# Kernel tuning notes

Measured on AMD Instinct MI355X. Metric: run time of the kernel, lower is better.

## Reference

```python
import jax, jax.numpy as jnp
import numpy as np

B, T, D = 2, 128, 1024
H, R, Dk, Dv = 8, 8, 64, 64


def setup_inputs() -> dict:
    key = jax.random.key(0)
    ks = jax.random.split(key, 11)
    w = lambda k, shp: jax.random.normal(k, shp, dtype=jnp.float32) * 0.02
    return {
        "hidden_states": jax.random.normal(ks[0], (B, T, D), dtype=jnp.float32),
        "Wq": w(ks[1], (D, H * Dk)),
        "Wk": w(ks[2], (D, H * Dk)),
        "Wv": w(ks[3], (D, H * Dv)),
        "Wb": w(ks[4], (D, H * R)),
        "Wtg": w(ks[5], (D, H * R)),
        "mode_logits": jax.random.normal(ks[6], (H, R), dtype=jnp.float32) * 0.1,
        "log_decay": jax.random.normal(ks[7], (H, R), dtype=jnp.float32) * 0.1,
        "omega_log_scale": jax.random.normal(ks[8], (H, R), dtype=jnp.float32) * 0.1,
        "Wg": w(ks[9], (D, H * Dv)),
        "Wo": w(ks[10], (H * Dv, D)),
    }


def _forward(x, Wq, Wk, Wv, Wb, Wtg, mode_logits, log_decay, omega_log_scale, Wg, Wo):
    b, t, _ = x.shape
    # projections
    q = (x @ Wq).reshape(b, t, H, Dk)
    k = (x @ Wk).reshape(b, t, H, Dk)
    v = (x @ Wv).reshape(b, t, H, Dv)
    beta = jax.nn.sigmoid((x @ Wb).reshape(b, t, H, R))
    tg = jax.nn.sigmoid((x @ Wtg).reshape(b, t, H, R))
    # spectral mode parameters
    pair_idx = jnp.arange(0, Dk, 2, dtype=jnp.float32)
    inv_freq = 1.0 / (10000.0 ** (pair_idx / Dk))            # [Dk/2]
    omega = jnp.exp(omega_log_scale)[..., None] * inv_freq    # [H,R,Dk/2]
    omega_full = jnp.repeat(omega, 2, axis=-1)                # [H,R,Dk] (repeat_interleave)
    cos_w = jnp.cos(omega_full)[None, :, :, None, :]          # [1,H,R,1,Dk]
    sin_w = jnp.sin(omega_full)[None, :, :, None, :]
    rho = jnp.exp(-jax.nn.softplus(log_decay))                # [H,R]
    mode_w = jax.nn.softmax(mode_logits, axis=-1)             # [H,R]

    # time-major for scan
    qT = jnp.moveaxis(q, 1, 0)
    kT = jnp.moveaxis(k, 1, 0)
    vT = jnp.moveaxis(v, 1, 0)
    betaT = jnp.moveaxis(beta, 1, 0)
    tgT = jnp.moveaxis(tg, 1, 0)

    def step(carry, xs):
        sr, si = carry                      # [B,H,R,Dv,Dk] each
        q_t, k_t, v_t, b_t, g_t = xs
        decay = (g_t * rho)[..., None, None]            # [B,H,R,1,1]
        rot_r = decay * (cos_w * sr - sin_w * si)
        rot_i = decay * (sin_w * sr + cos_w * si)
        pred = jnp.einsum('bhrvk,bhk->bhrv', rot_r, k_t)
        err = v_t[:, :, None, :] - pred                  # [B,H,R,Dv]
        write = err[..., None] * k_t[:, :, None, None, :]
        sr_new = rot_r + b_t[..., None, None] * write
        read = jnp.einsum('bhrvk,bhk->bhrv', sr_new, q_t)
        y = jnp.einsum('bhrv,hr->bhv', read, mode_w)     # [B,H,Dv]
        return (sr_new, rot_i), y

    s0 = jnp.zeros((b, H, R, Dv, Dk), dtype=x.dtype)
    _, ys = jax.lax.scan(step, (s0, s0), (qT, kT, vT, betaT, tgT))
    o = jnp.moveaxis(ys, 0, 1)                           # [B,T,H,Dv]
    gate = jax.nn.sigmoid((x @ Wg).reshape(b, t, H, Dv))
    o = (o * gate).reshape(b, t, H * Dv)
    return o @ Wo


def reference(hidden_states, Wq, Wk, Wv, Wb, Wtg, mode_logits, log_decay,
              omega_log_scale, Wg, Wo):
    return _forward(hidden_states, Wq, Wk, Wv, Wb, Wtg, mode_logits,
                    log_decay, omega_log_scale, Wg, Wo)
```

## Files before the change

kernel.cpp:

```cpp
#include <hip/hip_runtime.h>
#include <math.h>

#define T_ 128
#define NPROJ 2176
#define CH 32

typedef __attribute__((ext_vector_type(8))) short short8;
typedef __attribute__((ext_vector_type(4))) float float4v;
typedef __attribute__((ext_vector_type(2))) float float2v;

__device__ __forceinline__ ushort f2bf(float x) {
    unsigned u = __float_as_uint(x);
    u += 0x7FFF + ((u >> 16) & 1);
    return (ushort)(u >> 16);
}

__global__ __launch_bounds__(256) void prep_kernel(
    const float* __restrict__ x,
    const float* __restrict__ Wq, const float* __restrict__ Wk,
    const float* __restrict__ Wv, const float* __restrict__ Wb,
    const float* __restrict__ Wtg, const float* __restrict__ Wg,
    const float* __restrict__ Wo,
    const float* __restrict__ mode_logits, const float* __restrict__ log_decay,
    const float* __restrict__ ols,
    float* __restrict__ cosw, float* __restrict__ sinw,
    float* __restrict__ rho, float* __restrict__ modew,
    ushort* __restrict__ xb, ushort* __restrict__ wtb, ushort* __restrict__ wotb,
    float* __restrict__ Acomb)
{
    __shared__ ushort tile[64][68];
    const int blk = blockIdx.x, tid = threadIdx.x;
    if (blk < 16) {
        int idx = blk * 256 + tid;
        if (idx >= 64 * 64) return;
        int t = idx >> 6;
        int k = idx & 63;
        int h = t >> 3;
        if (k == 0) {
            float ld = log_decay[t];
            rho[t] = 1.0f / (1.0f + expf(ld));
            float m = -1e30f;
            for (int i = 0; i < 8; i++) m = fmaxf(m, mode_logits[h * 8 + i]);
            float sum = 0.0f;
            for (int i = 0; i < 8; i++) sum += expf(mode_logits[h * 8 + i] - m);
            modew[t] = expf(mode_logits[t] - m) / sum;
        }
        float osc = expf(ols[t]);
        int p = k >> 1;
        float invf = expf(-((float)(2 * p) / 64.0f) * logf(10000.0f));
        float w = osc * invf;
        cosw[idx] = cosf(w);
        sinw[idx] = sinf(w);
        return;
    }
    if (blk < 80) {
        int base = (blk - 16) * 4096 + tid * 16;
        float4 f0 = *(const float4*)&x[base];
        float4 f1 = *(const float4*)&x[base + 4];
        float4 f2 = *(const float4*)&x[base + 8];
        float4 f3 = *(const float4*)&x[base + 12];
        short8 o0, o1;
        o0[0]=f2bf(f0.x); o0[1]=f2bf(f0.y); o0[2]=f2bf(f0.z); o0[3]=f2bf(f0.w);
        o0[4]=f2bf(f1.x); o0[5]=f2bf(f1.y); o0[6]=f2bf(f1.z); o0[7]=f2bf(f1.w);
        o1[0]=f2bf(f2.x); o1[1]=f2bf(f2.y); o1[2]=f2bf(f2.z); o1[3]=f2bf(f2.w);
        o1[4]=f2bf(f3.x); o1[5]=f2bf(f3.y); o1[6]=f2bf(f3.z); o1[7]=f2bf(f3.w);
        *(short8*)&xb[base] = o0;
        *(short8*)&xb[base + 8] = o1;
        return;
    }
    if (blk >= 752) {
        int base = (blk - 752) * 4096 + tid * 16;
        float4 z = make_float4(0.f, 0.f, 0.f, 0.f);
        *(float4*)&Acomb[base] = z;
        *(float4*)&Acomb[base + 4] = z;
        *(float4*)&Acomb[base + 8] = z;
        *(float4*)&Acomb[base + 12] = z;
        return;
    }
    const float* src; int ld, c0, n0, k0, ldd; ushort* dst;
    if (blk < 624) {
        int b3 = blk - 80; int nt = b3 >> 4, kt = b3 & 15;
        n0 = nt * 64; k0 = kt * 64;
        if (n0 < 512)       { src = Wq;  c0 = n0;        ld = 512; }
        else if (n0 < 1024) { src = Wk;  c0 = n0 - 512;  ld = 512; }
        else if (n0 < 1536) { src = Wv;  c0 = n0 - 1024; ld = 512; }
        else if (n0 < 1600) { src = Wb;  c0 = n0 - 1536; ld = 64;  }
        else if (n0 < 1664) { src = Wtg; c0 = n0 - 1600; ld = 64;  }
        else                { src = Wg;  c0 = n0 - 1664; ld = 512; }
        dst = wtb; ldd = 1024;
    } else {
        int b4 = blk - 624; int nt = b4 >> 3, kt = b4 & 7;
        n0 = nt * 64; k0 = kt * 64;
        src = Wo; c0 = n0; ld = 1024; dst = wotb; ldd = 512;
    }
    #pragma unroll
    for (int rep = 0; rep < 4; rep++) {
        int k = rep * 16 + (tid >> 4);
        int nc = (tid & 15) * 4;
        float4 f = *(const float4*)&src[(size_t)(k0 + k) * ld + c0 + nc];
        tile[nc + 0][k] = f2bf(f.x);
        tile[nc + 1][k] = f2bf(f.y);
        tile[nc + 2][k] = f2bf(f.z);
        tile[nc + 3][k] = f2bf(f.w);
    }
    __syncthreads();
    #pragma unroll
    for (int rep = 0; rep < 4; rep++) {
        int n = rep * 16 + (tid >> 4);
        int kc = (tid & 15) * 4;
        uint2 u = *(const uint2*)&tile[n][kc];
        *(uint2*)&dst[(size_t)(n0 + n) * ldd + k0 + kc] = u;
    }
}

__global__ __launch_bounds__(256, 2) void proj_mfma(const ushort* __restrict__ Ab,
        const ushort* __restrict__ BTb, float* __restrict__ proj)
{
    __shared__ ushort sA[2][64][40];
    __shared__ ushort sB[2][64][40];
    const int n0 = blockIdx.x * 64, m0 = blockIdx.y * 64;
    const int tid = threadIdx.x;
    const int lane = tid & 63, w = tid >> 6;
    const int wm = w & 1, wn = w >> 1;
    const int l16 = lane & 15, quad = lane >> 4;
    const int srow = tid >> 2, skq = (tid & 3) * 8;
    const ushort* Ag = Ab + (size_t)(m0 + srow) * 1024 + skq;
    const ushort* Bg = BTb + (size_t)(n0 + srow) * 1024 + skq;
    short8 ra = *(const short8*)Ag;
    short8 rb = *(const short8*)Bg;
    float4v acc00 = {0,0,0,0}, acc01 = {0,0,0,0}, acc10 = {0,0,0,0}, acc11 = {0,0,0,0};
    for (int kt = 0; kt < 32; kt++) {
        const int cb = kt & 1;
        *(short8*)&sA[cb][srow][skq] = ra;
        *(short8*)&sB[cb][srow][skq] = rb;
        __syncthreads();
        if (kt + 1 < 32) {
            ra = *(const short8*)(Ag + (kt + 1) * 32);
            rb = *(const short8*)(Bg + (kt + 1) * 32);
        }
        short8 a0 = *(const short8*)&sA[cb][wm * 32 + l16][quad * 8];
        short8 a1 = *(const short8*)&sA[cb][wm * 32 + 16 + l16][quad * 8];
        short8 b0 = *(const short8*)&sB[cb][wn * 32 + l16][quad * 8];
        short8 b1 = *(const short8*)&sB[cb][wn * 32 + 16 + l16][quad * 8];
        acc00 = __builtin_amdgcn_mfma_f32_16x16x32_bf16(a0, b0, acc00, 0, 0, 0);
        acc01 = __builtin_amdgcn_mfma_f32_16x16x32_bf16(a0, b1, acc01, 0, 0, 0);
        acc10 = __builtin_amdgcn_mfma_f32_16x16x32_bf16(a1, b0, acc10, 0, 0, 0);
        acc11 = __builtin_amdgcn_mfma_f32_16x16x32_bf16(a1, b1, acc11, 0, 0, 0);
    }
    const bool sig = (n0 >= 1536);
    const int colb = n0 + wn * 32 + l16;
    const int rowb = m0 + wm * 32 + quad * 4;
    #pragma unroll
    for (int r2 = 0; r2 < 4; r2++) {
        float v00 = acc00[r2], v01 = acc01[r2], v10 = acc10[r2], v11 = acc11[r2];
        if (sig) {
            v00 = 1.0f / (1.0f + expf(-v00));
            v01 = 1.0f / (1.0f + expf(-v01));
            v10 = 1.0f / (1.0f + expf(-v10));
            v11 = 1.0f / (1.0f + expf(-v11));
        }
        proj[(size_t)(rowb + r2) * NPROJ + colb] = v00;
        proj[(size_t)(rowb + r2) * NPROJ + colb + 16] = v01;
        proj[(size_t)(rowb + 16 + r2) * NPROJ + colb] = v10;
        proj[(size_t)(rowb + 16 + r2) * NPROJ + colb + 16] = v11;
    }
}

template<int CTRL>
__device__ __forceinline__ float dpp_add(float x) {
    int xi = __float_as_int(x);
    int yi = __builtin_amdgcn_update_dpp(xi, xi, CTRL, 0xF, 0xF, false);
    return x + __int_as_float(yi);
}

__global__ __launch_bounds__(256, 2) void scan_kernel(const float* __restrict__ proj,
        const float* __restrict__ cosw, const float* __restrict__ sinw,
        const float* __restrict__ rho, const float* __restrict__ modew,
        float* __restrict__ Acomb)
{
    __shared__ float qk[2][CH][128];
    __shared__ float vbuf[2][CH][16];
    __shared__ float gbuf[2][CH][16];
    __shared__ float sc4[2][CH][4];

    const int bi = blockIdx.x;
    const int s  = bi & 3;
    const int hr = (bi >> 2) & 63;
    const int b  = bi >> 8;
    const int h = hr >> 3, r = hr & 7;
    const int tid = threadIdx.x;
    const int vl = tid >> 4;
    const int kl = tid & 15;

    float2v cw0, cw1, sw0, sw1;
    cw0.x = cosw[hr * 64 + kl * 4 + 0]; cw0.y = cosw[hr * 64 + kl * 4 + 1];
    cw1.x = cosw[hr * 64 + kl * 4 + 2]; cw1.y = cosw[hr * 64 + kl * 4 + 3];
    sw0.x = sinw[hr * 64 + kl * 4 + 0]; sw0.y = sinw[hr * 64 + kl * 4 + 1];
    sw1.x = sinw[hr * 64 + kl * 4 + 2]; sw1.y = sinw[hr * 64 + kl * 4 + 3];
    const float rho_hr = rho[hr];
    const float mw = modew[hr];
    float2v sr0 = {0,0}, sr1 = {0,0}, si0 = {0,0}, si1 = {0,0};

    const float* pb = proj + (size_t)b * T_ * NPROJ;
    const int qbase = h * 64;
    const int kbase = 512 + h * 64;
    const int vbase = 1024 + h * 64 + s * 16;
    const int gbase = 1664 + h * 64 + s * 16;
    const int boff  = 1536 + h * 8 + r;
    const int goff  = 1600 + h * 8 + r;

    auto stage = [&](int t0, int nb) {
        #pragma unroll
        for (int rep = 0; rep < 4; rep++) {
            int idx = rep * 256 + tid;
            int t = idx >> 5, sub = idx & 31;
            const float* row = pb + (size_t)(t0 + t) * NPROJ;
            float4 val = *(const float4*)(row + (sub < 16 ? qbase + sub * 4
                                                          : kbase + (sub - 16) * 4));
            *(float4*)&qk[nb][t][sub * 4] = val;
        }
        if (tid < 128) {
            int t = tid >> 2, sub = tid & 3;
            *(float4*)&vbuf[nb][t][sub * 4] =
                *(const float4*)(pb + (size_t)(t0 + t) * NPROJ + vbase + sub * 4);
        } else {
            int t = (tid - 128) >> 2, sub = tid & 3;
            *(float4*)&gbuf[nb][t][sub * 4] =
                *(const float4*)(pb + (size_t)(t0 + t) * NPROJ + gbase + sub * 4);
        }
        if (tid < CH)            sc4[nb][tid][0]      = pb[(size_t)(t0 + tid) * NPROJ + boff];
        else if (tid < 2 * CH)   sc4[nb][tid - CH][1] = pb[(size_t)(t0 + tid - CH) * NPROJ + goff];
    };

    stage(0, 0);
    __syncthreads();

    float* dst = Acomb + ((size_t)b * 128) * 512 + h * 64 + s * 16 + vl;

    for (int c = 0; c < T_ / CH; c++) {
        const int cb = c & 1;
        {
            int t = tid >> 3, j = tid & 7;
            float4 ka = *(const float4*)&qk[cb][t][64 + j * 8];
            float4 kb4 = *(const float4*)&qk[cb][t][64 + j * 8 + 4];
            float4 qa = *(const float4*)&qk[cb][t][j * 8];
            float4 qb4 = *(const float4*)&qk[cb][t][j * 8 + 4];
            float p = ka.x * qa.x + ka.y * qa.y + ka.z * qa.z + ka.w * qa.w
                    + kb4.x * qb4.x + kb4.y * qb4.y + kb4.z * qb4.z + kb4.w * qb4.w;
            p = dpp_add<0xB1>(p);
            p = dpp_add<0x4E>(p);
            p = dpp_add<0x141>(p);
            if (j == 0) sc4[cb][t][2] = p;
        }
        __syncthreads();
        if (c + 1 < T_ / CH) stage((c + 1) * CH, (c + 1) & 1);

        #pragma unroll 4
        for (int t = 0; t < CH; t++) {
            float4 kf = *(const float4*)&qk[cb][t][64 + kl * 4];
            float4 qf = *(const float4*)&qk[cb][t][kl * 4];
            float4 sv = *(const float4*)&sc4[cb][t][0];
            const float vv = vbuf[cb][t][vl];
            const float gate = gbuf[cb][t][vl];

            const float decay = sv.y * rho_hr;
            float2v k0; k0.x = kf.x; k0.y = kf.y;
            float2v k1; k1.x = kf.z; k1.y = kf.w;
            float2v q0; q0.x = qf.x; q0.y = qf.y;
            float2v q1; q1.x = qf.z; q1.y = qf.w;

            float2v t1 = cw0 * sr0 - sw0 * si0;
            float2v u1 = sw0 * sr0 + cw0 * si0;
            float2v t2 = cw1 * sr1 - sw1 * si1;
            float2v u2 = sw1 * sr1 + cw1 * si1;
            float2v d2; d2.x = decay; d2.y = decay;
            float2v rr0 = d2 * t1, rr1 = d2 * t2;
            si0 = d2 * u1; si1 = d2 * u2;

            float2v pk2 = rr0 * k0 + rr1 * k1;
            float2v pq2 = rr0 * q0 + rr1 * q1;
            float pk = pk2.x + pk2.y;
            float pq = pq2.x + pq2.y;
            pk = dpp_add<0xB1>(pk);  pq = dpp_add<0xB1>(pq);
            pk = dpp_add<0x4E>(pk);  pq = dpp_add<0x4E>(pq);
            pk = dpp_add<0x141>(pk); pq = dpp_add<0x141>(pq);
            pk = dpp_add<0x140>(pk); pq = dpp_add<0x140>(pq);

            const float sc = sv.x * (vv - pk);
            float2v sc2; sc2.x = sc; sc2.y = sc;
            sr0 = rr0 + sc2 * k0;
            sr1 = rr1 + sc2 * k1;
            const float rp = pq + sc * sv.z;
            if (kl == 0) atomicAdd(dst + (size_t)(c * CH + t) * 512, mw * rp * gate);
        }
        __syncthreads();
    }
}

__global__ __launch_bounds__(256, 2) void out_mfma(const float* __restrict__ Af,
        const ushort* __restrict__ BTb, float* __restrict__ C)
{
    __shared__ ushort sA[2][64][40];
    __shared__ ushort sB[2][64][40];
    const int n0 = blockIdx.x * 64, m0 = blockIdx.y * 64;
    const int tid = threadIdx.x;
    const int lane = tid & 63, w = tid >> 6;
    const int wm = w & 1, wn = w >> 1;
    const int l16 = lane & 15, quad = lane >> 4;
    const int srow = tid >> 2, skq = (tid & 3) * 8;
    const float* Ag = Af + (size_t)(m0 + srow) * 512 + skq;
    const ushort* Bg = BTb + (size_t)(n0 + srow) * 512 + skq;
    float4 fa0 = *(const float4*)Ag;
    float4 fa1 = *(const float4*)(Ag + 4);
    short8 rb = *(const short8*)Bg;
    float4v acc00 = {0,0,0,0}, acc01 = {0,0,0,0}, acc10 = {0,0,0,0}, acc11 = {0,0,0,0};
    for (int kt = 0; kt < 16; kt++) {
        const int cb = kt & 1;
        short8 ra;
        ra[0]=f2bf(fa0.x); ra[1]=f2bf(fa0.y); ra[2]=f2bf(fa0.z); ra[3]=f2bf(fa0.w);
        ra[4]=f2bf(fa1.x); ra[5]=f2bf(fa1.y); ra[6]=f2bf(fa1.z); ra[7]=f2bf(fa1.w);
        *(short8*)&sA[cb][srow][skq] = ra;
        *(short8*)&sB[cb][srow][skq] = rb;
        __syncthreads();
        if (kt + 1 < 16) {
            fa0 = *(const float4*)(Ag + (kt + 1) * 32);
            fa1 = *(const float4*)(Ag + (kt + 1) * 32 + 4);
            rb = *(const short8*)(Bg + (kt + 1) * 32);
        }
        short8 a0 = *(const short8*)&sA[cb][wm * 32 + l16][quad * 8];
        short8 a1 = *(const short8*)&sA[cb][wm * 32 + 16 + l16][quad * 8];
        short8 b0 = *(const short8*)&sB[cb][wn * 32 + l16][quad * 8];
        short8 b1 = *(const short8*)&sB[cb][wn * 32 + 16 + l16][quad * 8];
        acc00 = __builtin_amdgcn_mfma_f32_16x16x32_bf16(a0, b0, acc00, 0, 0, 0);
        acc01 = __builtin_amdgcn_mfma_f32_16x16x32_bf16(a0, b1, acc01, 0, 0, 0);
        acc10 = __builtin_amdgcn_mfma_f32_16x16x32_bf16(a1, b0, acc10, 0, 0, 0);
        acc11 = __builtin_amdgcn_mfma_f32_16x16x32_bf16(a1, b1, acc11, 0, 0, 0);
    }
    const int colb = n0 + wn * 32 + l16;
    const int rowb = m0 + wm * 32 + quad * 4;
    #pragma unroll
    for (int r2 = 0; r2 < 4; r2++) {
        C[(size_t)(rowb + r2) * 1024 + colb] = acc00[r2];
        C[(size_t)(rowb + r2) * 1024 + colb + 16] = acc01[r2];
        C[(size_t)(rowb + 16 + r2) * 1024 + colb] = acc10[r2];
        C[(size_t)(rowb + 16 + r2) * 1024 + colb + 16] = acc11[r2];
    }
}

extern "C" void kernel_launch(void* const* d_in, const int* in_sizes, int n_in,
                              void* d_out, int out_size, void* d_ws, size_t ws_size,
                              hipStream_t stream) {
    const float* x   = (const float*)d_in[0];
    const float* Wq  = (const float*)d_in[1];
    const float* Wk  = (const float*)d_in[2];
    const float* Wv  = (const float*)d_in[3];
    const float* Wb  = (const float*)d_in[4];
    const float* Wtg = (const float*)d_in[5];
    const float* ml  = (const float*)d_in[6];
    const float* ldc = (const float*)d_in[7];
    const float* ols = (const float*)d_in[8];
    const float* Wg  = (const float*)d_in[9];
    const float* Wo  = (const float*)d_in[10];
    float* out = (float*)d_out;

    float* ws = (float*)d_ws;
    float* proj    = ws;
    float* cosw    = proj + 256 * NPROJ;
    float* sinw    = cosw + 4096;
    float* rho     = sinw + 4096;
    float* modew   = rho + 64;
    ushort* xb     = (ushort*)(modew + 64);
    ushort* wotb   = (ushort*)((float*)xb + 131072);
    float*  Acomb  = (float*)wotb + 262144;
    ushort* wtb    = (ushort*)(Acomb + 131072);

    prep_kernel<<<784, 256, 0, stream>>>(x, Wq, Wk, Wv, Wb, Wtg, Wg, Wo,
                                         ml, ldc, ols, cosw, sinw, rho, modew,
                                         xb, wtb, wotb, Acomb);
    proj_mfma<<<dim3(34, 4), 256, 0, stream>>>(xb, wtb, proj);
    scan_kernel<<<512, 256, 0, stream>>>(proj, cosw, sinw, rho, modew, Acomb);
    out_mfma<<<dim3(16, 4), 256, 0, stream>>>(Acomb, wotb, out);
}
```

Baseline: 140.2 us.

## Fuse four kernels into one cooperative persistent kernel with grid syncs

```diff
diff --git a/kernel.cpp b/kernel.cpp
--- a/kernel.cpp
+++ b/kernel.cpp
@@ -1,5 +1,8 @@
 #include <hip/hip_runtime.h>
+#include <hip/hip_cooperative_groups.h>
 #include <math.h>
+
+namespace cg = cooperative_groups;
 
 #define T_ 128
 #define NPROJ 2176
@@ -13,157 +16,6 @@
     unsigned u = __float_as_uint(x);
     u += 0x7FFF + ((u >> 16) & 1);
     return (ushort)(u >> 16);
-}
-
-__global__ __launch_bounds__(256) void prep_kernel(
-    const float* __restrict__ x,
-    const float* __restrict__ Wq, const float* __restrict__ Wk,
-    const float* __restrict__ Wv, const float* __restrict__ Wb,
-    const float* __restrict__ Wtg, const float* __restrict__ Wg,
-    const float* __restrict__ Wo,
-    const float* __restrict__ mode_logits, const float* __restrict__ log_decay,
-    const float* __restrict__ ols,
-    float* __restrict__ cosw, float* __restrict__ sinw,
-    float* __restrict__ rho, float* __restrict__ modew,
-    ushort* __restrict__ xb, ushort* __restrict__ wtb, ushort* __restrict__ wotb,
-    float* __restrict__ Acomb)
-{
-    __shared__ ushort tile[64][68];
-    const int blk = blockIdx.x, tid = threadIdx.x;
-    if (blk < 16) {
-        int idx = blk * 256 + tid;
-        if (idx >= 64 * 64) return;
-        int t = idx >> 6;
-        int k = idx & 63;
-        int h = t >> 3;
-        if (k == 0) {
-            float ld = log_decay[t];
-            rho[t] = 1.0f / (1.0f + expf(ld));
-            float m = -1e30f;
-            for (int i = 0; i < 8; i++) m = fmaxf(m, mode_logits[h * 8 + i]);
-            float sum = 0.0f;
-            for (int i = 0; i < 8; i++) sum += expf(mode_logits[h * 8 + i] - m);
-            modew[t] = expf(mode_logits[t] - m) / sum;
-        }
-        float osc = expf(ols[t]);
-        int p = k >> 1;
-        float invf = expf(-((float)(2 * p) / 64.0f) * logf(10000.0f));
-        float w = osc * invf;
-        cosw[idx] = cosf(w);
-        sinw[idx] = sinf(w);
-        return;
-    }
-    if (blk < 80) {
-        int base = (blk - 16) * 4096 + tid * 16;
-        float4 f0 = *(const float4*)&x[base];
-        float4 f1 = *(const float4*)&x[base + 4];
-        float4 f2 = *(const float4*)&x[base + 8];
-        float4 f3 = *(const float4*)&x[base + 12];
-        short8 o0, o1;
-        o0[0]=f2bf(f0.x); o0[1]=f2bf(f0.y); o0[2]=f2bf(f0.z); o0[3]=f2bf(f0.w);
-        o0[4]=f2bf(f1.x); o0[5]=f2bf(f1.y); o0[6]=f2bf(f1.z); o0[7]=f2bf(f1.w);
-        o1[0]=f2bf(f2.x); o1[1]=f2bf(f2.y); o1[2]=f2bf(f2.z); o1[3]=f2bf(f2.w);
-        o1[4]=f2bf(f3.x); o1[5]=f2bf(f3.y); o1[6]=f2bf(f3.z); o1[7]=f2bf(f3.w);
-        *(short8*)&xb[base] = o0;
-        *(short8*)&xb[base + 8] = o1;
-        return;
-    }
-    if (blk >= 752) {
-        int base = (blk - 752) * 4096 + tid * 16;
-        float4 z = make_float4(0.f, 0.f, 0.f, 0.f);
-        *(float4*)&Acomb[base] = z;
-        *(float4*)&Acomb[base + 4] = z;
-        *(float4*)&Acomb[base + 8] = z;
-        *(float4*)&Acomb[base + 12] = z;
-        return;
-    }
-    const float* src; int ld, c0, n0, k0, ldd; ushort* dst;
-    if (blk < 624) {
-        int b3 = blk - 80; int nt = b3 >> 4, kt = b3 & 15;
-        n0 = nt * 64; k0 = kt * 64;
-        if (n0 < 512)       { src = Wq;  c0 = n0;        ld = 512; }
-        else if (n0 < 1024) { src = Wk;  c0 = n0 - 512;  ld = 512; }
-        else if (n0 < 1536) { src = Wv;  c0 = n0 - 1024; ld = 512; }
-        else if (n0 < 1600) { src = Wb;  c0 = n0 - 1536; ld = 64;  }
-        else if (n0 < 1664) { src = Wtg; c0 = n0 - 1600; ld = 64;  }
-        else                { src = Wg;  c0 = n0 - 1664; ld = 512; }
-        dst = wtb; ldd = 1024;
-    } else {
-        int b4 = blk - 624; int nt = b4 >> 3, kt = b4 & 7;
-        n0 = nt * 64; k0 = kt * 64;
-        src = Wo; c0 = n0; ld = 1024; dst = wotb; ldd = 512;
-    }
-    #pragma unroll
-    for (int rep = 0; rep < 4; rep++) {
-        int k = rep * 16 + (tid >> 4);
-        int nc = (tid & 15) * 4;
-        float4 f = *(const float4*)&src[(size_t)(k0 + k) * ld + c0 + nc];
-        tile[nc + 0][k] = f2bf(f.x);
-        tile[nc + 1][k] = f2bf(f.y);
-        tile[nc + 2][k] = f2bf(f.z);
-        tile[nc + 3][k] = f2bf(f.w);
-    }
-    __syncthreads();
-    #pragma unroll
-    for (int rep = 0; rep < 4; rep++) {
-        int n = rep * 16 + (tid >> 4);
-        int kc = (tid & 15) * 4;
-        uint2 u = *(const uint2*)&tile[n][kc];
-        *(uint2*)&dst[(size_t)(n0 + n) * ldd + k0 + kc] = u;
-    }
-}
-
-__global__ __launch_bounds__(256, 2) void proj_mfma(const ushort* __restrict__ Ab,
-        const ushort* __restrict__ BTb, float* __restrict__ proj)
-{
-    __shared__ ushort sA[2][64][40];
-    __shared__ ushort sB[2][64][40];
-    const int n0 = blockIdx.x * 64, m0 = blockIdx.y * 64;
-    const int tid = threadIdx.x;
-    const int lane = tid & 63, w = tid >> 6;
-    const int wm = w & 1, wn = w >> 1;
-    const int l16 = lane & 15, quad = lane >> 4;
-    const int srow = tid >> 2, skq = (tid & 3) * 8;
-    const ushort* Ag = Ab + (size_t)(m0 + srow) * 1024 + skq;
-    const ushort* Bg = BTb + (size_t)(n0 + srow) * 1024 + skq;
-    short8 ra = *(const short8*)Ag;
-    short8 rb = *(const short8*)Bg;
-    float4v acc00 = {0,0,0,0}, acc01 = {0,0,0,0}, acc10 = {0,0,0,0}, acc11 = {0,0,0,0};
-    for (int kt = 0; kt < 32; kt++) {
-        const int cb = kt & 1;
-        *(short8*)&sA[cb][srow][skq] = ra;
-        *(short8*)&sB[cb][srow][skq] = rb;
-        __syncthreads();
-        if (kt + 1 < 32) {
-            ra = *(const short8*)(Ag + (kt + 1) * 32);
-            rb = *(const short8*)(Bg + (kt + 1) * 32);
-        }
-        short8 a0 = *(const short8*)&sA[cb][wm * 32 + l16][quad * 8];
-        short8 a1 = *(const short8*)&sA[cb][wm * 32 + 16 + l16][quad * 8];
-        short8 b0 = *(const short8*)&sB[cb][wn * 32 + l16][quad * 8];
-        short8 b1 = *(const short8*)&sB[cb][wn * 32 + 16 + l16][quad * 8];
-        acc00 = __builtin_amdgcn_mfma_f32_16x16x32_bf16(a0, b0, acc00, 0, 0, 0);
-        acc01 = __builtin_amdgcn_mfma_f32_16x16x32_bf16(a0, b1, acc01, 0, 0, 0);
-        acc10 = __builtin_amdgcn_mfma_f32_16x16x32_bf16(a1, b0, acc10, 0, 0, 0);
-        acc11 = __builtin_amdgcn_mfma_f32_16x16x32_bf16(a1, b1, acc11, 0, 0, 0);
-    }
-    const bool sig = (n0 >= 1536);
-    const int colb = n0 + wn * 32 + l16;
-    const int rowb = m0 + wm * 32 + quad * 4;
-    #pragma unroll
-    for (int r2 = 0; r2 < 4; r2++) {
-        float v00 = acc00[r2], v01 = acc01[r2], v10 = acc10[r2], v11 = acc11[r2];
-        if (sig) {
-            v00 = 1.0f / (1.0f + expf(-v00));
-            v01 = 1.0f / (1.0f + expf(-v01));
-            v10 = 1.0f / (1.0f + expf(-v10));
-            v11 = 1.0f / (1.0f + expf(-v11));
-        }
-        proj[(size_t)(rowb + r2) * NPROJ + colb] = v00;
-        proj[(size_t)(rowb + r2) * NPROJ + colb + 16] = v01;
-        proj[(size_t)(rowb + 16 + r2) * NPROJ + colb] = v10;
-        proj[(size_t)(rowb + 16 + r2) * NPROJ + colb + 16] = v11;
-    }
 }
 
 template<int CTRL>
@@ -173,211 +25,347 @@
     return x + __int_as_float(yi);
 }
 
-__global__ __launch_bounds__(256, 2) void scan_kernel(const float* __restrict__ proj,
-        const float* __restrict__ cosw, const float* __restrict__ sinw,
-        const float* __restrict__ rho, const float* __restrict__ modew,
-        float* __restrict__ Acomb)
+struct KParams {
+    const float *x, *Wq, *Wk, *Wv, *Wb, *Wtg, *ml, *ldc, *ols, *Wg, *Wo;
+    float *cosw, *sinw, *rho, *modew, *proj, *Acomb, *out;
+    ushort *xb, *wtb, *wotb;
+};
+
+struct SmemGemm { ushort sA[2][64][40]; ushort sB[2][64][40]; };
+struct SmemScan { float qk[2][CH][128]; float vbuf[2][CH][16];
+                  float gbuf[2][CH][16]; float sc4[2][CH][4]; };
+struct SmemPrep { ushort tile[64][68]; };
+union Smem { SmemGemm g; SmemScan s; SmemPrep p; };
+
+__global__ __launch_bounds__(256, 2) void mega_kernel(KParams P)
 {
-    __shared__ float qk[2][CH][128];
-    __shared__ float vbuf[2][CH][16];
-    __shared__ float gbuf[2][CH][16];
-    __shared__ float sc4[2][CH][4];
-
-    const int bi = blockIdx.x;
-    const int s  = bi & 3;
-    const int hr = (bi >> 2) & 63;
-    const int b  = bi >> 8;
-    const int h = hr >> 3, r = hr & 7;
+    __shared__ Smem sm;
+    cg::grid_group grid = cg::this_grid();
+    const int blk = blockIdx.x;
     const int tid = threadIdx.x;
-    const int vl = tid >> 4;
-    const int kl = tid & 15;
-
-    float2v cw0, cw1, sw0, sw1;
-    cw0.x = cosw[hr * 64 + kl * 4 + 0]; cw0.y = cosw[hr * 64 + kl * 4 + 1];
-    cw1.x = cosw[hr * 64 + kl * 4 + 2]; cw1.y = cosw[hr * 64 + kl * 4 + 3];
-    sw0.x = sinw[hr * 64 + kl * 4 + 0]; sw0.y = sinw[hr * 64 + kl * 4 + 1];
-    sw1.x = sinw[hr * 64 + kl * 4 + 2]; sw1.y = sinw[hr * 64 + kl * 4 + 3];
-    const float rho_hr = rho[hr];
-    const float mw = modew[hr];
-    float2v sr0 = {0,0}, sr1 = {0,0}, si0 = {0,0}, si1 = {0,0};
-
-    const float* pb = proj + (size_t)b * T_ * NPROJ;
-    const int qbase = h * 64;
-    const int kbase = 512 + h * 64;
-    const int vbase = 1024 + h * 64 + s * 16;
-    const int gbase = 1664 + h * 64 + s * 16;
-    const int boff  = 1536 + h * 8 + r;
-    const int goff  = 1600 + h * 8 + r;
-
-    auto stage = [&](int t0, int nb) {
+
+    for (int u = blk; u < 784; u += 512) {
+        __syncthreads();
+        if (u < 16) {
+            int idx = u * 256 + tid;
+            if (idx < 64 * 64) {
+                int t = idx >> 6;
+                int k = idx & 63;
+                int h = t >> 3;
+                if (k == 0) {
+                    float ld = P.ldc[t];
+                    P.rho[t] = 1.0f / (1.0f + expf(ld));
+                    float m = -1e30f;
+                    for (int i = 0; i < 8; i++) m = fmaxf(m, P.ml[h * 8 + i]);
+                    float sum = 0.0f;
+                    for (int i = 0; i < 8; i++) sum += expf(P.ml[h * 8 + i] - m);
+                    P.modew[t] = expf(P.ml[t] - m) / sum;
+                }
+                float osc = expf(P.ols[t]);
+                int p = k >> 1;
+                float invf = expf(-((float)(2 * p) / 64.0f) * logf(10000.0f));
+                float w = osc * invf;
+                P.cosw[idx] = cosf(w);
+                P.sinw[idx] = sinf(w);
+            }
+        } else if (u < 80) {
+            int base = (u - 16) * 4096 + tid * 16;
+            float4 f0 = *(const float4*)&P.x[base];
+            float4 f1 = *(const float4*)&P.x[base + 4];
+            float4 f2 = *(const float4*)&P.x[base + 8];
+            float4 f3 = *(const float4*)&P.x[base + 12];
+            short8 o0, o1;
+            o0[0]=f2bf(f0.x); o0[1]=f2bf(f0.y); o0[2]=f2bf(f0.z); o0[3]=f2bf(f0.w);
+            o0[4]=f2bf(f1.x); o0[5]=f2bf(f1.y); o0[6]=f2bf(f1.z); o0[7]=f2bf(f1.w);
+            o1[0]=f2bf(f2.x); o1[1]=f2bf(f2.y); o1[2]=f2bf(f2.z); o1[3]=f2bf(f2.w);
+            o1[4]=f2bf(f3.x); o1[5]=f2bf(f3.y); o1[6]=f2bf(f3.z); o1[7]=f2bf(f3.w);
+            *(short8*)&P.xb[base] = o0;
+            *(short8*)&P.xb[base + 8] = o1;
+        } else if (u < 752) {
+            const float* src; int ld, c0, n0, k0, ldd; ushort* dst;
+            if (u < 624) {
+                int b3 = u - 80; int nt = b3 >> 4, kt = b3 & 15;
+                n0 = nt * 64; k0 = kt * 64;
+                if (n0 < 512)       { src = P.Wq;  c0 = n0;        ld = 512; }
+                else if (n0 < 1024) { src = P.Wk;  c0 = n0 - 512;  ld = 512; }
+                else if (n0 < 1536) { src = P.Wv;  c0 = n0 - 1024; ld = 512; }
+                else if (n0 < 1600) { src = P.Wb;  c0 = n0 - 1536; ld = 64;  }
+                else if (n0 < 1664) { src = P.Wtg; c0 = n0 - 1600; ld = 64;  }
+                else                { src = P.Wg;  c0 = n0 - 1664; ld = 512; }
+                dst = P.wtb; ldd = 1024;
+            } else {
+                int b4 = u - 624; int nt = b4 >> 3, kt = b4 & 7;
+                n0 = nt * 64; k0 = kt * 64;
+                src = P.Wo; c0 = n0; ld = 1024; dst = P.wotb; ldd = 512;
+            }
+            #pragma unroll
+            for (int rep = 0; rep < 4; rep++) {
+                int k = rep * 16 + (tid >> 4);
+                int nc = (tid & 15) * 4;
+                float4 f = *(const float4*)&src[(size_t)(k0 + k) * ld + c0 + nc];
+                sm.p.tile[nc + 0][k] = f2bf(f.x);
+                sm.p.tile[nc + 1][k] = f2bf(f.y);
+                sm.p.tile[nc + 2][k] = f2bf(f.z);
+                sm.p.tile[nc + 3][k] = f2bf(f.w);
+            }
+            __syncthreads();
+            #pragma unroll
+            for (int rep = 0; rep < 4; rep++) {
+                int n = rep * 16 + (tid >> 4);
+                int kc = (tid & 15) * 4;
+                uint2 uu = *(const uint2*)&sm.p.tile[n][kc];
+                *(uint2*)&dst[(size_t)(n0 + n) * ldd + k0 + kc] = uu;
+            }
+        } else {
+            int base = (u - 752) * 4096 + tid * 16;
+            float4 z = make_float4(0.f, 0.f, 0.f, 0.f);
+            *(float4*)&P.Acomb[base] = z;
+            *(float4*)&P.Acomb[base + 4] = z;
+            *(float4*)&P.Acomb[base + 8] = z;
+            *(float4*)&P.Acomb[base + 12] = z;
+        }
+    }
+    grid.sync();
+
+    if (blk < 136) {
+        const int n0 = (blk % 34) * 64, m0 = (blk / 34) * 64;
+        const int lane = tid & 63, w = tid >> 6;
+        const int wm = w & 1, wn = w >> 1;
+        const int l16 = lane & 15, quad = lane >> 4;
+        const int srow = tid >> 2, skq = (tid & 3) * 8;
+        const ushort* Ag = P.xb + (size_t)(m0 + srow) * 1024 + skq;
+        const ushort* Bg = P.wtb + (size_t)(n0 + srow) * 1024 + skq;
+        short8 ra = *(const short8*)Ag;
+        short8 rb = *(const short8*)Bg;
+        float4v acc00 = {0,0,0,0}, acc01 = {0,0,0,0}, acc10 = {0,0,0,0}, acc11 = {0,0,0,0};
+        for (int kt = 0; kt < 32; kt++) {
+            const int cb = kt & 1;
+            *(short8*)&sm.g.sA[cb][srow][skq] = ra;
+            *(short8*)&sm.g.sB[cb][srow][skq] = rb;
+            __syncthreads();
+            if (kt + 1 < 32) {
+                ra = *(const short8*)(Ag + (kt + 1) * 32);
+                rb = *(const short8*)(Bg + (kt + 1) * 32);
+            }
+            short8 a0 = *(const short8*)&sm.g.sA[cb][wm * 32 + l16][quad * 8];
+            short8 a1 = *(const short8*)&sm.g.sA[cb][wm * 32 + 16 + l16][quad * 8];
+            short8 b0 = *(const short8*)&sm.g.sB[cb][wn * 32 + l16][quad * 8];
+            short8 b1 = *(const short8*)&sm.g.sB[cb][wn * 32 + 16 + l16][quad * 8];
+            acc00 = __builtin_amdgcn_mfma_f32_16x16x32_bf16(a0, b0, acc00, 0, 0, 0);
+            acc01 = __builtin_amdgcn_mfma_f32_16x16x32_bf16(a0, b1, acc01, 0, 0, 0);
+            acc10 = __builtin_amdgcn_mfma_f32_16x16x32_bf16(a1, b0, acc10, 0, 0, 0);
+            acc11 = __builtin_amdgcn_mfma_f32_16x16x32_bf16(a1, b1, acc11, 0, 0, 0);
+        }
+        const bool sig = (n0 >= 1536);
+        const int colb = n0 + wn * 32 + l16;
+        const int rowb = m0 + wm * 32 + quad * 4;
         #pragma unroll
-        for (int rep = 0; rep < 4; rep++) {
-            int idx = rep * 256 + tid;
-            int t = idx >> 5, sub = idx & 31;
-            const float* row = pb + (size_t)(t0 + t) * NPROJ;
-            float4 val = *(const float4*)(row + (sub < 16 ? qbase + sub * 4
-                                                          : kbase + (sub - 16) * 4));
-            *(float4*)&qk[nb][t][sub * 4] = val;
-        }
-        if (tid < 128) {
-            int t = tid >> 2, sub = tid & 3;
-            *(float4*)&vbuf[nb][t][sub * 4] =
-                *(const float4*)(pb + (size_t)(t0 + t) * NPROJ + vbase + sub * 4);
-        } else {
-            int t = (tid - 128) >> 2, sub = tid & 3;
-            *(float4*)&gbuf[nb][t][sub * 4] =
-                *(const float4*)(pb + (size_t)(t0 + t) * NPROJ + gbase + sub * 4);
-        }
-        if (tid < CH)            sc4[nb][tid][0]      = pb[(size_t)(t0 + tid) * NPROJ + boff];
-        else if (tid < 2 * CH)   sc4[nb][tid - CH][1] = pb[(size_t)(t0 + tid - CH) * NPROJ + goff];
-    };
-
-    stage(0, 0);
-    __syncthreads();
-
-    float* dst = Acomb + ((size_t)b * 128) * 512 + h * 64 + s * 16 + vl;
-
-    for (int c = 0; c < T_ / CH; c++) {
-        const int cb = c & 1;
-        {
-            int t = tid >> 3, j = tid & 7;
-            float4 ka = *(const float4*)&qk[cb][t][64 + j * 8];
-            float4 kb4 = *(const float4*)&qk[cb][t][64 + j * 8 + 4];
-            float4 qa = *(const float4*)&qk[cb][t][j * 8];
-            float4 qb4 = *(const float4*)&qk[cb][t][j * 8 + 4];
-            float p = ka.x * qa.x + ka.y * qa.y + ka.z * qa.z + ka.w * qa.w
-                    + kb4.x * qb4.x + kb4.y * qb4.y + kb4.z * qb4.z + kb4.w * qb4.w;
-            p = dpp_add<0xB1>(p);
-            p = dpp_add<0x4E>(p);
-            p = dpp_add<0x141>(p);
-            if (j == 0) sc4[cb][t][2] = p;
-        }
+        for (int r2 = 0; r2 < 4; r2++) {
+            float v00 = acc00[r2], v01 = acc01[r2], v10 = acc10[r2], v11 = acc11[r2];
+            if (sig) {
+                v00 = 1.0f / (1.0f + expf(-v00));
+                v01 = 1.0f / (1.0f + expf(-v01));
+                v10 = 1.0f / (1.0f + expf(-v10));
+                v11 = 1.0f / (1.0f + expf(-v11));
+            }
+            P.proj[(size_t)(rowb + r2) * NPROJ + colb] = v00;
+            P.proj[(size_t)(rowb + r2) * NPROJ + colb + 16] = v01;
+            P.proj[(size_t)(rowb + 16 + r2) * NPROJ + colb] = v10;
+            P.proj[(size_t)(rowb + 16 + r2) * NPROJ + colb + 16] = v11;
+        }
+    }
+    grid.sync();
+
+    {
+        const int s  = blk & 3;
+        const int hr = (blk >> 2) & 63;
+        const int b  = blk >> 8;
+        const int h = hr >> 3, r = hr & 7;
+        const int vl = tid >> 4;
+        const int kl = tid & 15;
+
+        float2v cw0, cw1, sw0, sw1;
+        cw0.x = P.cosw[hr * 64 + kl * 4 + 0]; cw0.y = P.cosw[hr * 64 + kl * 4 + 1];
+        cw1.x = P.cosw[hr * 64 + kl * 4 + 2]; cw1.y = P.cosw[hr * 64 + kl * 4 + 3];
+        sw0.x = P.sinw[hr * 64 + kl * 4 + 0]; sw0.y = P.sinw[hr * 64 + kl * 4 + 1];
+        sw1.x = P.sinw[hr * 64 + kl * 4 + 2]; sw1.y = P.sinw[hr * 64 + kl * 4 + 3];
+        const float rho_hr = P.rho[hr];
+        const float mw = P.modew[hr];
+        float2v sr0 = {0,0}, sr1 = {0,0}, si0 = {0,0}, si1 = {0,0};
+
+        const float* pb = P.proj + (size_t)b * T_ * NPROJ;
+        const int qbase = h * 64;
+        const int kbase = 512 + h * 64;
+        const int vbase = 1024 + h * 64 + s * 16;
+        const int gbase = 1664 + h * 64 + s * 16;
+        const int boff  = 1536 + h * 8 + r;
+        const int goff  = 1600 + h * 8 + r;
+
+        auto stage = [&](int t0, int nb) {
+            #pragma unroll
+            for (int rep = 0; rep < 4; rep++) {
+                int idx = rep * 256 + tid;
+                int t = idx >> 5, sub = idx & 31;
+                const float* row = pb + (size_t)(t0 + t) * NPROJ;
+                float4 val = *(const float4*)(row + (sub < 16 ? qbase + sub * 4
+                                                              : kbase + (sub - 16) * 4));
+                *(float4*)&sm.s.qk[nb][t][sub * 4] = val;
+            }
+            if (tid < 128) {
+                int t = tid >> 2, sub = tid & 3;
+                *(float4*)&sm.s.vbuf[nb][t][sub * 4] =
+                    *(const float4*)(pb + (size_t)(t0 + t) * NPROJ + vbase + sub * 4);
+            } else {
+                int t = (tid - 128) >> 2, sub = tid & 3;
+                *(float4*)&sm.s.gbuf[nb][t][sub * 4] =
+                    *(const float4*)(pb + (size_t)(t0 + t) * NPROJ + gbase + sub * 4);
+            }
+            if (tid < CH)            sm.s.sc4[nb][tid][0]      = pb[(size_t)(t0 + tid) * NPROJ + boff];
+            else if (tid < 2 * CH)   sm.s.sc4[nb][tid - CH][1] = pb[(size_t)(t0 + tid - CH) * NPROJ + goff];
+        };
+
         __syncthreads();
-        if (c + 1 < T_ / CH) stage((c + 1) * CH, (c + 1) & 1);
-
-        #pragma unroll 4
-        for (int t = 0; t < CH; t++) {
-            float4 kf = *(const float4*)&qk[cb][t][64 + kl * 4];
-            float4 qf = *(const float4*)&qk[cb][t][kl * 4];
-            float4 sv = *(const float4*)&sc4[cb][t][0];
-            const float vv = vbuf[cb][t][vl];
-            const float gate = gbuf[cb][t][vl];
-
-            const float decay = sv.y * rho_hr;
-            float2v k0; k0.x = kf.x; k0.y = kf.y;
-            float2v k1; k1.x = kf.z; k1.y = kf.w;
-            float2v q0; q0.x = qf.x; q0.y = qf.y;
-            float2v q1; q1.x = qf.z; q1.y = qf.w;
-
-            float2v t1 = cw0 * sr0 - sw0 * si0;
-            float2v u1 = sw0 * sr0 + cw0 * si0;
-            float2v t2 = cw1 * sr1 - sw1 * si1;
-            float2v u2 = sw1 * sr1 + cw1 * si1;
-            float2v d2; d2.x = decay; d2.y = decay;
-            float2v rr0 = d2 * t1, rr1 = d2 * t2;
-            si0 = d2 * u1; si1 = d2 * u2;
-
-            float2v pk2 = rr0 * k0 + rr1 * k1;
-            float2v pq2 = rr0 * q0 + rr1 * q1;
-            float pk = pk2.x + pk2.y;
-            float pq = pq2.x + pq2.y;
-            pk = dpp_add<0xB1>(pk);  pq = dpp_add<0xB1>(pq);
-            pk = dpp_add<0x4E>(pk);  pq = dpp_add<0x4E>(pq);
-            pk = dpp_add<0x141>(pk); pq = dpp_add<0x141>(pq);
-            pk = dpp_add<0x140>(pk); pq = dpp_add<0x140>(pq);
-
-            const float sc = sv.x * (vv - pk);
-            float2v sc2; sc2.x = sc; sc2.y = sc;
-            sr0 = rr0 + sc2 * k0;
-            sr1 = rr1 + sc2 * k1;
-            const float rp = pq + sc * sv.z;
-            if (kl == 0) atomicAdd(dst + (size_t)(c * CH + t) * 512, mw * rp * gate);
-        }
+        stage(0, 0);
         __syncthreads();
+
+        float* dst = P.Acomb + ((size_t)b * 128) * 512 + h * 64 + s * 16 + vl;
+
+        for (int c = 0; c < T_ / CH; c++) {
+            const int cb = c & 1;
+            {
+                int t = tid >> 3, j = tid & 7;
+                float4 ka = *(const float4*)&sm.s.qk[cb][t][64 + j * 8];
+                float4 kb4 = *(const float4*)&sm.s.qk[cb][t][64 + j * 8 + 4];
+                float4 qa = *(const float4*)&sm.s.qk[cb][t][j * 8];
+                float4 qb4 = *(const float4*)&sm.s.qk[cb][t][j * 8 + 4];
+                float p = ka.x * qa.x + ka.y * qa.y + ka.z * qa.z + ka.w * qa.w
+                        + kb4.x * qb4.x + kb4.y * qb4.y + kb4.z * qb4.z + kb4.w * qb4.w;
+                p = dpp_add<0xB1>(p);
+                p = dpp_add<0x4E>(p);
+                p = dpp_add<0x141>(p);
+                if (j == 0) sm.s.sc4[cb][t][2] = p;
+            }
+            __syncthreads();
+            if (c + 1 < T_ / CH) stage((c + 1) * CH, (c + 1) & 1);
+
+            #pragma unroll 4
+            for (int t = 0; t < CH; t++) {
+                float4 kf = *(const float4*)&sm.s.qk[cb][t][64 + kl * 4];
+                float4 qf = *(const float4*)&sm.s.qk[cb][t][kl * 4];
+                float4 sv = *(const float4*)&sm.s.sc4[cb][t][0];
+                const float vv = sm.s.vbuf[cb][t][vl];
+                const float gate = sm.s.gbuf[cb][t][vl];
+
+                const float decay = sv.y * rho_hr;
+                float2v k0; k0.x = kf.x; k0.y = kf.y;
+                float2v k1; k1.x = kf.z; k1.y = kf.w;
+                float2v q0; q0.x = qf.x; q0.y = qf.y;
+                float2v q1; q1.x = qf.z; q1.y = qf.w;
+
+                float2v t1 = cw0 * sr0 - sw0 * si0;
+                float2v u1 = sw0 * sr0 + cw0 * si0;
+                float2v t2 = cw1 * sr1 - sw1 * si1;
+                float2v u2 = sw1 * sr1 + cw1 * si1;
+                float2v d2; d2.x = decay; d2.y = decay;
+                float2v rr0 = d2 * t1, rr1 = d2 * t2;
+                si0 = d2 * u1; si1 = d2 * u2;
+
+                float2v pk2 = rr0 * k0 + rr1 * k1;
+                float2v pq2 = rr0 * q0 + rr1 * q1;
+                float pk = pk2.x + pk2.y;
+                float pq = pq2.x + pq2.y;
+                pk = dpp_add<0xB1>(pk);  pq = dpp_add<0xB1>(pq);
+                pk = dpp_add<0x4E>(pk);  pq = dpp_add<0x4E>(pq);
+                pk = dpp_add<0x141>(pk); pq = dpp_add<0x141>(pq);
+                pk = dpp_add<0x140>(pk); pq = dpp_add<0x140>(pq);
+
+                const float sc = sv.x * (vv - pk);
+                float2v sc2; sc2.x = sc; sc2.y = sc;
+                sr0 = rr0 + sc2 * k0;
+                sr1 = rr1 + sc2 * k1;
+                const float rp = pq + sc * sv.z;
+                if (kl == 0) atomicAdd(dst + (size_t)(c * CH + t) * 512, mw * rp * gate);
+            }
+            __syncthreads();
+        }
     }
-}
-
-__global__ __launch_bounds__(256, 2) void out_mfma(const float* __restrict__ Af,
-        const ushort* __restrict__ BTb, float* __restrict__ C)
-{
-    __shared__ ushort sA[2][64][40];
-    __shared__ ushort sB[2][64][40];
-    const int n0 = blockIdx.x * 64, m0 = blockIdx.y * 64;
-    const int tid = threadIdx.x;
-    const int lane = tid & 63, w = tid >> 6;
-    const int wm = w & 1, wn = w >> 1;
-    const int l16 = lane & 15, quad = lane >> 4;
-    const int srow = tid >> 2, skq = (tid & 3) * 8;
-    const float* Ag = Af + (size_t)(m0 + srow) * 512 + skq;
-    const ushort* Bg = BTb + (size_t)(n0 + srow) * 512 + skq;
-    float4 fa0 = *(const float4*)Ag;
-    float4 fa1 = *(const float4*)(Ag + 4);
-    short8 rb = *(const short8*)Bg;
-    float4v acc00 = {0,0,0,0}, acc01 = {0,0,0,0}, acc10 = {0,0,0,0}, acc11 = {0,0,0,0};
-    for (int kt = 0; kt < 16; kt++) {
-        const int cb = kt & 1;
-        short8 ra;
-        ra[0]=f2bf(fa0.x); ra[1]=f2bf(fa0.y); ra[2]=f2bf(fa0.z); ra[3]=f2bf(fa0.w);
-        ra[4]=f2bf(fa1.x); ra[5]=f2bf(fa1.y); ra[6]=f2bf(fa1.z); ra[7]=f2bf(fa1.w);
-        *(short8*)&sA[cb][srow][skq] = ra;
-        *(short8*)&sB[cb][srow][skq] = rb;
-        __syncthreads();
-        if (kt + 1 < 16) {
-            fa0 = *(const float4*)(Ag + (kt + 1) * 32);
-            fa1 = *(const float4*)(Ag + (kt + 1) * 32 + 4);
-            rb = *(const short8*)(Bg + (kt + 1) * 32);
-        }
-        short8 a0 = *(const short8*)&sA[cb][wm * 32 + l16][quad * 8];
-        short8 a1 = *(const short8*)&sA[cb][wm * 32 + 16 + l16][quad * 8];
-        short8 b0 = *(const short8*)&sB[cb][wn * 32 + l16][quad * 8];
-        short8 b1 = *(const short8*)&sB[cb][wn * 32 + 16 + l16][quad * 8];
-        acc00 = __builtin_amdgcn_mfma_f32_16x16x32_bf16(a0, b0, acc00, 0, 0, 0);
-        acc01 = __builtin_amdgcn_mfma_f32_16x16x32_bf16(a0, b1, acc01, 0, 0, 0);
-        acc10 = __builtin_amdgcn_mfma_f32_16x16x32_bf16(a1, b0, acc10, 0, 0, 0);
-        acc11 = __builtin_amdgcn_mfma_f32_16x16x32_bf16(a1, b1, acc11, 0, 0, 0);
-    }
-    const int colb = n0 + wn * 32 + l16;
-    const int rowb = m0 + wm * 32 + quad * 4;
-    #pragma unroll
-    for (int r2 = 0; r2 < 4; r2++) {
-        C[(size_t)(rowb + r2) * 1024 + colb] = acc00[r2];
-        C[(size_t)(rowb + r2) * 1024 + colb + 16] = acc01[r2];
-        C[(size_t)(rowb + 16 + r2) * 1024 + colb] = acc10[r2];
-        C[(size_t)(rowb + 16 + r2) * 1024 + colb + 16] = acc11[r2];
+    grid.sync();
+
+    if (blk < 64) {
+        const int n0 = (blk % 16) * 64, m0 = (blk / 16) * 64;
+        const int lane = tid & 63, w = tid >> 6;
+        const int wm = w & 1, wn = w >> 1;
+        const int l16 = lane & 15, quad = lane >> 4;
+        const int srow = tid >> 2, skq = (tid & 3) * 8;
+        const float* Ag = P.Acomb + (size_t)(m0 + srow) * 512 + skq;
+        const ushort* Bg = P.wotb + (size_t)(n0 + srow) * 512 + skq;
+        float4 fa0 = *(const float4*)Ag;
+        float4 fa1 = *(const float4*)(Ag + 4);
+        short8 rb = *(const short8*)Bg;
+        float4v acc00 = {0,0,0,0}, acc01 = {0,0,0,0}, acc10 = {0,0,0,0}, acc11 = {0,0,0,0};
+        for (int kt = 0; kt < 16; kt++) {
+            const int cb = kt & 1;
+            short8 ra;
+            ra[0]=f2bf(fa0.x); ra[1]=f2bf(fa0.y); ra[2]=f2bf(fa0.z); ra[3]=f2bf(fa0.w);
+            ra[4]=f2bf(fa1.x); ra[5]=f2bf(fa1.y); ra[6]=f2bf(fa1.z); ra[7]=f2bf(fa1.w);
+            *(short8*)&sm.g.sA[cb][srow][skq] = ra;
+            *(short8*)&sm.g.sB[cb][srow][skq] = rb;
+            __syncthreads();
+            if (kt + 1 < 16) {
+                fa0 = *(const float4*)(Ag + (kt + 1) * 32);
+                fa1 = *(const float4*)(Ag + (kt + 1) * 32 + 4);
+                rb = *(const short8*)(Bg + (kt + 1) * 32);
+            }
+            short8 a0 = *(const short8*)&sm.g.sA[cb][wm * 32 + l16][quad * 8];
+            short8 a1 = *(const short8*)&sm.g.sA[cb][wm * 32 + 16 + l16][quad * 8];
+            short8 b0 = *(const short8*)&sm.g.sB[cb][wn * 32 + l16][quad * 8];
+            short8 b1 = *(const short8*)&sm.g.sB[cb][wn * 32 + 16 + l16][quad * 8];
+            acc00 = __builtin_amdgcn_mfma_f32_16x16x32_bf16(a0, b0, acc00, 0, 0, 0);
+            acc01 = __builtin_amdgcn_mfma_f32_16x16x32_bf16(a0, b1, acc01, 0, 0, 0);
+            acc10 = __builtin_amdgcn_mfma_f32_16x16x32_bf16(a1, b0, acc10, 0, 0, 0);
+            acc11 = __builtin_amdgcn_mfma_f32_16x16x32_bf16(a1, b1, acc11, 0, 0, 0);
+        }
+        const int colb = n0 + wn * 32 + l16;
+        const int rowb = m0 + wm * 32 + quad * 4;
+        #pragma unroll
+        for (int r2 = 0; r2 < 4; r2++) {
+            P.out[(size_t)(rowb + r2) * 1024 + colb] = acc00[r2];
+            P.out[(size_t)(rowb + r2) * 1024 + colb + 16] = acc01[r2];
+            P.out[(size_t)(rowb + 16 + r2) * 1024 + colb] = acc10[r2];
+            P.out[(size_t)(rowb + 16 + r2) * 1024 + colb + 16] = acc11[r2];
+        }
     }
 }
 
 extern "C" void kernel_launch(void* const* d_in, const int* in_sizes, int n_in,
                               void* d_out, int out_size, void* d_ws, size_t ws_size,
                               hipStream_t stream) {
-    const float* x   = (const float*)d_in[0];
-    const float* Wq  = (const float*)d_in[1];
-    const float* Wk  = (const float*)d_in[2];
-    const float* Wv  = (const float*)d_in[3];
-    const float* Wb  = (const float*)d_in[4];
-    const float* Wtg = (const float*)d_in[5];
-    const float* ml  = (const float*)d_in[6];
-    const float* ldc = (const float*)d_in[7];
-    const float* ols = (const float*)d_in[8];
-    const float* Wg  = (const float*)d_in[9];
-    const float* Wo  = (const float*)d_in[10];
-    float* out = (float*)d_out;
-
     float* ws = (float*)d_ws;
-    float* proj    = ws;
-    float* cosw    = proj + 256 * NPROJ;
-    float* sinw    = cosw + 4096;
-    float* rho     = sinw + 4096;
-    float* modew   = rho + 64;
-    ushort* xb     = (ushort*)(modew + 64);
-    ushort* wotb   = (ushort*)((float*)xb + 131072);
-    float*  Acomb  = (float*)wotb + 262144;
-    ushort* wtb    = (ushort*)(Acomb + 131072);
-
-    prep_kernel<<<784, 256, 0, stream>>>(x, Wq, Wk, Wv, Wb, Wtg, Wg, Wo,
-                                         ml, ldc, ols, cosw, sinw, rho, modew,
-                                         xb, wtb, wotb, Acomb);
-    proj_mfma<<<dim3(34, 4), 256, 0, stream>>>(xb, wtb, proj);
-    scan_kernel<<<512, 256, 0, stream>>>(proj, cosw, sinw, rho, modew, Acomb);
-    out_mfma<<<dim3(16, 4), 256, 0, stream>>>(Acomb, wotb, out);
+    KParams P;
+    P.x   = (const float*)d_in[0];
+    P.Wq  = (const float*)d_in[1];
+    P.Wk  = (const float*)d_in[2];
+    P.Wv  = (const float*)d_in[3];
+    P.Wb  = (const float*)d_in[4];
+    P.Wtg = (const float*)d_in[5];
+    P.ml  = (const float*)d_in[6];
+    P.ldc = (const float*)d_in[7];
+    P.ols = (const float*)d_in[8];
+    P.Wg  = (const float*)d_in[9];
+    P.Wo  = (const float*)d_in[10];
+    P.out = (float*)d_out;
+
+    P.proj  = ws;
+    P.cosw  = P.proj + 256 * NPROJ;
+    P.sinw  = P.cosw + 4096;
+    P.rho   = P.sinw + 4096;
+    P.modew = P.rho + 64;
+    P.xb    = (ushort*)(P.modew + 64);
+    P.wotb  = (ushort*)((float*)P.xb + 131072);
+    P.Acomb = (float*)P.wotb + 262144;
+    P.wtb   = (ushort*)(P.Acomb + 131072);
+
+    void* args[] = { &P };
+    hipLaunchCooperativeKernel((void*)mega_kernel, dim3(512), dim3(256),
+                               args, 0, stream);
 }
```

Result: slower. 332.6 us (+137.2%).
